# Performance work log

Hardware: AMD Instinct MI355X
Metric: run time of the kernel (lower is better)

The kernel has to match this reference:

```python
import jax, jax.numpy as jnp
import numpy as np
import math

B, T, C = 16, 1029, 1024
H, D = 16, 64  # n_heads, head_dim
NPH = NPW = 32  # 32x32 patch grid -> 1024 patch tokens
ROPE_BASE = 100.0


def _rope_cos_sin():
    # DINOv3 patch-center coordinates in [-1, 1]
    ch = (np.arange(0.5, NPH, dtype=np.float32) / NPH)
    cw = (np.arange(0.5, NPW, dtype=np.float32) / NPW)
    coords = np.stack(np.meshgrid(ch, cw, indexing='ij'), axis=-1).reshape(-1, 2)  # [N,2]
    coords = 2.0 * coords - 1.0
    inv_freq = 1.0 / ROPE_BASE ** np.arange(0, 1, 4.0 / D, dtype=np.float32)  # [D/4]
    angles = 2.0 * math.pi * coords[:, :, None] * inv_freq[None, None, :]  # [N,2,D/4]
    angles = angles.reshape(-1, D // 2)  # [N, D/2]
    angles = np.tile(angles, (1, 2))  # [N, D]
    return jnp.asarray(np.cos(angles)), jnp.asarray(np.sin(angles))


def setup_inputs() -> dict:
    key = jax.random.key(0)
    ks = jax.random.split(key, 6)
    s = 1.0 / math.sqrt(C)
    cos, sin = _rope_cos_sin()
    return {
        'x': jax.random.normal(ks[0], (B, T, C), jnp.float32),
        'Wqkv': jax.random.normal(ks[1], (C, 3 * C), jnp.float32) * s,
        'bqkv': jax.random.normal(ks[2], (3 * C,), jnp.float32) * 0.02,
        'Wout': jax.random.normal(ks[3], (C, C), jnp.float32) * s,
        'bout': jax.random.normal(ks[4], (C,), jnp.float32) * 0.02,
        'cos': cos,
        'sin': sin,
        'num_prefix': 5,  # 1 CLS + 4 registers
    }


def _rotate_half(t):
    t1, t2 = jnp.split(t, 2, axis=-1)
    return jnp.concatenate((-t2, t1), axis=-1)


def reference(x, Wqkv, bqkv, Wout, bout, cos, sin, num_prefix):
    Bx, Tx, Cx = x.shape
    qkv = x @ Wqkv + bqkv  # [B,T,3C]
    q, k, v = jnp.split(qkv, 3, axis=-1)
    to_heads = lambda t: t.reshape(Bx, Tx, H, D).transpose(0, 2, 1, 3)  # [B,H,T,D]
    q, k, v = to_heads(q), to_heads(k), to_heads(v)

    # RoPE on patch tokens only (skip CLS/register prefix)
    qp = q[:, :, num_prefix:] * cos + _rotate_half(q[:, :, num_prefix:]) * sin
    kp = k[:, :, num_prefix:] * cos + _rotate_half(k[:, :, num_prefix:]) * sin
    q = jnp.concatenate((q[:, :, :num_prefix], qp), axis=2)
    k = jnp.concatenate((k[:, :, :num_prefix], kp), axis=2)

    scale = 1.0 / math.sqrt(D)
    attn = jax.nn.softmax(jnp.einsum('bhqd,bhkd->bhqk', q, k) * scale, axis=-1)
    y = jnp.einsum('bhqk,bhkd->bhqd', attn, v)  # [B,H,T,D]
    y = y.transpose(0, 2, 1, 3).reshape(Bx, Tx, Cx)
    return y @ Wout + bout
```

## Files before the change

### kernel.cpp

```cpp
#include <hip/hip_runtime.h>
#include <hip/hip_bf16.h>
#include <stdint.h>

typedef __bf16 bf16;
typedef bf16 bf16x8 __attribute__((ext_vector_type(8)));
typedef bf16 bf16x4 __attribute__((ext_vector_type(4)));
typedef float f32x4 __attribute__((ext_vector_type(4)));

#define DEV static __device__ __forceinline__

constexpr int Bc = 16, Tc = 1029, Cc = 1024, Hc = 16, Dc = 64;
constexpr int KPAD = 1088;
constexpr int QPAD = 1152;
constexpr int MPAD = 16512;
constexpr int NKT  = KPAD / 64;
constexpr int NVT  = KPAD / 32;

DEV void gload16(void* lds_dst, const void* gsrc) {
  __builtin_amdgcn_global_load_lds(
      (const __attribute__((address_space(1))) void*)gsrc,
      (__attribute__((address_space(3))) void*)lds_dst, 16, 0, 0);
}

__global__ __launch_bounds__(256) void cast_x(const float* __restrict__ x,
                                              bf16* __restrict__ xb) {
  const size_t i = ((size_t)blockIdx.x * 256 + threadIdx.x) * 8;
  const int row = (int)(i >> 10);
  bf16x8 o = {};
  if (row < Bc * Tc) {
    const float4* p = (const float4*)(x + i);
    float4 a = p[0], b = p[1];
    o[0] = (bf16)a.x; o[1] = (bf16)a.y; o[2] = (bf16)a.z; o[3] = (bf16)a.w;
    o[4] = (bf16)b.x; o[5] = (bf16)b.y; o[6] = (bf16)b.z; o[7] = (bf16)b.w;
  }
  *(bf16x8*)(xb + i) = o;
}

__global__ __launch_bounds__(256) void transpose_cast(const float* __restrict__ W,
                                                      bf16* __restrict__ Wt,
                                                      int rows, int cols) {
  __shared__ float tile[32][33];
  const int c0 = blockIdx.x * 32;
  const int r0 = blockIdx.y * 32;
  const int tr = threadIdx.x >> 5;
  const int tc = threadIdx.x & 31;
#pragma unroll
  for (int j = 0; j < 4; ++j)
    tile[tr + j * 8][tc] = W[(size_t)(r0 + tr + j * 8) * cols + c0 + tc];
  __syncthreads();
#pragma unroll
  for (int j = 0; j < 4; ++j)
    Wt[(size_t)(c0 + tr + j * 8) * rows + r0 + tc] = (bf16)tile[tc][tr + j * 8];
}

template <bool OUT_BF16>
__global__ __launch_bounds__(256) void gemm_bt(const bf16* __restrict__ A,
                                               const bf16* __restrict__ Bt,
                                               const float* __restrict__ bias,
                                               void* __restrict__ Cout,
                                               int N, int K, int Mlim) {
  constexpr int BM = 128, BN = 128, BK = 32;
  __shared__ bf16 As[2][BM * BK];
  __shared__ bf16 Bs[2][BN * BK];
  const int tid  = threadIdx.x;
  const int lane = tid & 63;
  const int wave = tid >> 6;
  const int g = lane >> 4;
  const int c = lane & 15;
  const int m0 = blockIdx.y * BM;
  const int n0 = blockIdx.x * BN;
  const int wm = (wave >> 1) * 64;
  const int wn = (wave & 1) * 64;

  auto stage = [&](int buf, int k0) {
#pragma unroll
    for (int j = 0; j < 2; ++j) {
      int idx = j * 256 + tid;
      int row = idx >> 2, ch = idx & 3;
      int sc = ((ch ^ ((row >> 1) & 3)) << 4);
      gload16((char*)&As[buf][0] + idx * 16,
              (const char*)(A + (size_t)(m0 + row) * K + k0) + sc);
    }
#pragma unroll
    for (int j = 0; j < 2; ++j) {
      int idx = j * 256 + tid;
      int row = idx >> 2, ch = idx & 3;
      int sc = ((ch ^ ((row >> 1) & 3)) << 4);
      gload16((char*)&Bs[buf][0] + idx * 16,
              (const char*)(Bt + (size_t)(n0 + row) * K + k0) + sc);
    }
  };

  f32x4 acc[4][4] = {};
  stage(0, 0);
  __syncthreads();
  const int nk = K / BK;
  for (int kt = 0; kt < nk; ++kt) {
    const int buf = kt & 1;
    if (kt + 1 < nk) stage(buf ^ 1, (kt + 1) * BK);
    bf16x8 af[4], bfr[4];
#pragma unroll
    for (int i = 0; i < 4; ++i) {
      const int ra = wm + i * 16 + c;
      const int rb = wn + i * 16 + c;
      af[i]  = *(const bf16x8*)((const char*)&As[buf][0] + ra * 64 +
                                (((g ^ ((ra >> 1) & 3)) << 4)));
      bfr[i] = *(const bf16x8*)((const char*)&Bs[buf][0] + rb * 64 +
                                (((g ^ ((rb >> 1) & 3)) << 4)));
    }
#pragma unroll
    for (int i = 0; i < 4; ++i)
#pragma unroll
      for (int j = 0; j < 4; ++j)
        acc[i][j] = __builtin_amdgcn_mfma_f32_16x16x32_bf16(af[i], bfr[j], acc[i][j], 0, 0, 0);
    __syncthreads();
  }

#pragma unroll
  for (int i = 0; i < 4; ++i) {
    const int mb = m0 + wm + i * 16 + g * 4;
#pragma unroll
    for (int j = 0; j < 4; ++j) {
      const int n = n0 + wn + j * 16 + c;
      const float bv = bias[n];
#pragma unroll
      for (int r = 0; r < 4; ++r) {
        const int m = mb + r;
        if (m < Mlim) {
          float v = acc[i][j][r] + bv;
          if constexpr (OUT_BF16)
            ((bf16*)Cout)[(size_t)m * N + n] = (bf16)v;
          else
            ((float*)Cout)[(size_t)m * N + n] = v;
        }
      }
    }
  }
}

__global__ __launch_bounds__(256) void rope_qk(const bf16* __restrict__ qkv,
                                               const float* __restrict__ cosT,
                                               const float* __restrict__ sinT,
                                               const int* __restrict__ npfx_p,
                                               bf16* __restrict__ Qh,
                                               bf16* __restrict__ Kh) {
  const int bt = blockIdx.x;
  const int b = bt / QPAD, t = bt % QPAD;
  const int h  = threadIdx.x >> 4;
  const int d0 = (threadIdx.x & 15) * 4;
  const size_t qoff = (((size_t)(b * Hc + h)) * QPAD + t) * Dc + d0;
  const size_t koff = (((size_t)(b * Hc + h)) * KPAD + t) * Dc + d0;
  if (t >= Tc) {
    bf16x4 z = {};
    *(bf16x4*)(Qh + qoff) = z;
    if (t < KPAD) *(bf16x4*)(Kh + koff) = z;
    return;
  }
  const int npfx = *npfx_p;
  const size_t inb = ((size_t)b * Tc + t) * 3072 + h * Dc;
  bf16x4 qv = *(const bf16x4*)(qkv + inb + d0);
  bf16x4 kv = *(const bf16x4*)(qkv + inb + 1024 + d0);
  float q[4], k[4];
#pragma unroll
  for (int u = 0; u < 4; ++u) { q[u] = (float)qv[u]; k[u] = (float)kv[u]; }
  if (t >= npfx) {
    const int p  = t - npfx;
    const int dp = (d0 < 32) ? d0 + 32 : d0 - 32;
    const float sgn = (d0 < 32) ? -1.f : 1.f;
    bf16x4 qp = *(const bf16x4*)(qkv + inb + dp);
    bf16x4 kp = *(const bf16x4*)(qkv + inb + 1024 + dp);
    float4 csv = *(const float4*)(cosT + (size_t)p * Dc + d0);
    float4 snv = *(const float4*)(sinT + (size_t)p * Dc + d0);
    float cs[4] = {csv.x, csv.y, csv.z, csv.w};
    float sn[4] = {snv.x, snv.y, snv.z, snv.w};
#pragma unroll
    for (int u = 0; u < 4; ++u) {
      q[u] = q[u] * cs[u] + sgn * (float)qp[u] * sn[u];
      k[u] = k[u] * cs[u] + sgn * (float)kp[u] * sn[u];
    }
  }
  bf16x4 qo, ko;
#pragma unroll
  for (int u = 0; u < 4; ++u) {
    qo[u] = (bf16)(q[u] * 0.18033688f);
    ko[u] = (bf16)k[u];
  }
  *(bf16x4*)(Qh + qoff) = qo;
  *(bf16x4*)(Kh + koff) = ko;
}

__global__ __launch_bounds__(256) void vtrans(const bf16* __restrict__ qkv,
                                              bf16* __restrict__ Vt) {
  __shared__ bf16 lds[64][40];
  const int blk = blockIdx.x;
  const int tt = blk % NVT;
  const int bh = blk / NVT;
  const int b = bh >> 4, h = bh & 15;
  const int t0 = tt * 32;
  const int tl = threadIdx.x >> 3;
  const int ch = threadIdx.x & 7;
  bf16x8 v = {};
  const int t = t0 + tl;
  if (t < Tc)
    v = *(const bf16x8*)(qkv + ((size_t)b * Tc + t) * 3072 + 2048 + h * Dc + ch * 8);
#pragma unroll
  for (int u = 0; u < 8; ++u) lds[ch * 8 + u][tl] = v[u];
  __syncthreads();
  const int d  = threadIdx.x >> 2;
  const int tc = threadIdx.x & 3;
  bf16x8 o = *(const bf16x8*)&lds[d][tc * 8];
  *(bf16x8*)(Vt + ((size_t)bh * Dc + d) * KPAD + t0 + tc * 8) = o;
}

__global__ __launch_bounds__(256, 3) void attn4(const bf16* __restrict__ Qh,
                                                const bf16* __restrict__ Kh,
                                                const bf16* __restrict__ Vt,
                                                bf16* __restrict__ y2d) {
  __shared__ bf16 Ks[2][64 * 64];
  __shared__ bf16 Vs[2][64 * 64];
  __shared__ bf16 Ps[4][32 * 64];
  const int bh = blockIdx.y;
  const int b = bh >> 4, h = bh & 15;
  const int tid = threadIdx.x;
  const int w = tid >> 6, lane = tid & 63;
  const int g = lane >> 4, c = lane & 15;
  const int q0 = blockIdx.x * 128 + w * 32;
  const bf16* Qb = Qh + (size_t)bh * QPAD * Dc;
  const bf16* Kb = Kh + (size_t)bh * KPAD * Dc;
  const bf16* Vb = Vt + (size_t)bh * Dc * KPAD;
  char* Pw = (char*)&Ps[w][0];

  auto stage = [&](int buf, int k0) {
#pragma unroll
    for (int j = 0; j < 2; ++j) {
      int idx = j * 256 + tid;
      int row = idx >> 3;
      int scb = ((idx & 7) << 4) ^ ((row & 7) << 4);
      gload16((char*)&Ks[buf][0] + idx * 16,
              (const char*)(Kb + (size_t)(k0 + row) * 64) + scb);
    }
#pragma unroll
    for (int j = 0; j < 2; ++j) {
      int idx = j * 256 + tid;
      int row = idx >> 3;
      int scb = ((idx & 7) << 4) ^ ((row & 7) << 4);
      gload16((char*)&Vs[buf][0] + idx * 16,
              (const char*)(Vb + (size_t)row * KPAD + k0) + scb);
    }
  };

  bf16x8 qf[2][2];
#pragma unroll
  for (int fm = 0; fm < 2; ++fm)
#pragma unroll
    for (int kc = 0; kc < 2; ++kc)
      qf[fm][kc] = *(const bf16x8*)(Qb + (size_t)(q0 + fm * 16 + c) * Dc + kc * 32 + g * 8);

  bf16x8 ones;
#pragma unroll
  for (int u = 0; u < 8; ++u) ones[u] = (bf16)1.0f;

  float mrun[2] = {-1e30f, -1e30f}, lrun[2] = {0.f, 0.f};
  f32x4 oacc[2][4] = {};

  stage(0, 0);
  __syncthreads();

  for (int kt = 0; kt < NKT; ++kt) {
    const int buf = kt & 1;
    const int k0 = kt * 64;
    if (kt + 1 < NKT) stage(buf ^ 1, (kt + 1) * 64);

    f32x4 st[4][2] = {};
    __builtin_amdgcn_s_setprio(1);
#pragma unroll
    for (int fn = 0; fn < 4; ++fn) {
      const int row = fn * 16 + c;
      const int sw = (row & 7) << 4;
#pragma unroll
      for (int kc = 0; kc < 2; ++kc) {
        bf16x8 kf = *(const bf16x8*)((const char*)&Ks[buf][0] + row * 128 +
                                     ((kc * 64 + g * 16) ^ sw));
#pragma unroll
        for (int fm = 0; fm < 2; ++fm)
          st[fn][fm] = __builtin_amdgcn_mfma_f32_16x16x32_bf16(kf, qf[fm][kc], st[fn][fm], 0, 0, 0);
      }
    }
    __builtin_amdgcn_s_setprio(0);

    if (k0 + 64 > Tc) {
#pragma unroll
      for (int fn = 0; fn < 4; ++fn)
#pragma unroll
        for (int r = 0; r < 4; ++r)
          if (k0 + fn * 16 + g * 4 + r >= Tc) {
            st[fn][0][r] = -1e30f;
            st[fn][1][r] = -1e30f;
          }
    }

    float mx[2];
#pragma unroll
    for (int fm = 0; fm < 2; ++fm) {
      float m0 = fmaxf(fmaxf(st[0][fm][0], st[0][fm][1]), fmaxf(st[0][fm][2], st[0][fm][3]));
      float m1 = fmaxf(fmaxf(st[1][fm][0], st[1][fm][1]), fmaxf(st[1][fm][2], st[1][fm][3]));
      float m2 = fmaxf(fmaxf(st[2][fm][0], st[2][fm][1]), fmaxf(st[2][fm][2], st[2][fm][3]));
      float m3 = fmaxf(fmaxf(st[3][fm][0], st[3][fm][1]), fmaxf(st[3][fm][2], st[3][fm][3]));
      float m = fmaxf(fmaxf(m0, m1), fmaxf(m2, m3));
      m = fmaxf(m, __shfl_xor(m, 16));
      m = fmaxf(m, __shfl_xor(m, 32));
      mx[fm] = m;
    }
    const bool ok = (mx[0] - mrun[0] <= 11.f) && (mx[1] - mrun[1] <= 11.f);
    if (!__all(ok)) {
#pragma unroll
      for (int fm = 0; fm < 2; ++fm) {
        const float mnew = fmaxf(mrun[fm], mx[fm]);
        const float al = __builtin_amdgcn_exp2f(mrun[fm] - mnew);
        mrun[fm] = mnew;
        lrun[fm] *= al;
#pragma unroll
        for (int fd = 0; fd < 4; ++fd) oacc[fm][fd] *= al;
      }
    }
#pragma unroll
    for (int fm = 0; fm < 2; ++fm) {
      const int row = fm * 16 + c;
      const int sw = (row & 7) << 4;
#pragma unroll
      for (int fn = 0; fn < 4; ++fn) {
        bf16x4 pv;
#pragma unroll
        for (int r = 0; r < 4; ++r)
          pv[r] = (bf16)__builtin_amdgcn_exp2f(st[fn][fm][r] - mrun[fm]);
        *(bf16x4*)(Pw + row * 128 + ((fn * 32 + g * 8) ^ sw)) = pv;
      }
    }

    bf16x8 pf[2][2];
    f32x4 ps2[2] = {};
#pragma unroll
    for (int fm = 0; fm < 2; ++fm) {
      const int row = fm * 16 + c;
      const int sw = (row & 7) << 4;
#pragma unroll
      for (int kc = 0; kc < 2; ++kc) {
        pf[fm][kc] = *(const bf16x8*)(Pw + row * 128 + ((kc * 64 + g * 16) ^ sw));
        ps2[fm] = __builtin_amdgcn_mfma_f32_16x16x32_bf16(ones, pf[fm][kc], ps2[fm], 0, 0, 0);
      }
    }
    __builtin_amdgcn_s_setprio(1);
#pragma unroll
    for (int fd = 0; fd < 4; ++fd) {
      const int row = fd * 16 + c;
      const int sw = (row & 7) << 4;
#pragma unroll
      for (int kc = 0; kc < 2; ++kc) {
        bf16x8 vf = *(const bf16x8*)((const char*)&Vs[buf][0] + row * 128 +
                                     ((kc * 64 + g * 16) ^ sw));
#pragma unroll
        for (int fm = 0; fm < 2; ++fm)
          oacc[fm][fd] = __builtin_amdgcn_mfma_f32_16x16x32_bf16(vf, pf[fm][kc], oacc[fm][fd], 0, 0, 0);
      }
    }
    __builtin_amdgcn_s_setprio(0);
#pragma unroll
    for (int fm = 0; fm < 2; ++fm) lrun[fm] += ps2[fm][0];
    __syncthreads();
  }

#pragma unroll
  for (int fm = 0; fm < 2; ++fm) {
    const int trow = q0 + fm * 16 + c;
    if (trow < Tc) {
      const float inv = 1.f / lrun[fm];
#pragma unroll
      for (int fd = 0; fd < 4; ++fd) {
        bf16x4 ov;
#pragma unroll
        for (int r = 0; r < 4; ++r) ov[r] = (bf16)(oacc[fm][fd][r] * inv);
        *(bf16x4*)(y2d + ((size_t)b * Tc + trow) * Cc + h * Dc + fd * 16 + g * 4) = ov;
      }
    }
  }
}

extern "C" void kernel_launch(void* const* d_in, const int* in_sizes, int n_in,
                              void* d_out, int out_size, void* d_ws, size_t ws_size,
                              hipStream_t stream) {
  const float* x    = (const float*)d_in[0];
  const float* Wqkv = (const float*)d_in[1];
  const float* bqkv = (const float*)d_in[2];
  const float* Wout = (const float*)d_in[3];
  const float* bout = (const float*)d_in[4];
  const float* cosT = (const float*)d_in[5];
  const float* sinT = (const float*)d_in[6];
  const int*   npfx = (const int*)d_in[7];

  char* ws = (char*)d_ws;
  size_t off = 0;
  auto alloc = [&](size_t bytes) {
    char* p = ws + off;
    off = (off + bytes + 255) & ~(size_t)255;
    return p;
  };
  bf16* xb  = (bf16*)alloc((size_t)MPAD * 1024 * 2);
  bf16* Wt1 = (bf16*)alloc((size_t)3072 * 1024 * 2);
  bf16* Wt2 = (bf16*)alloc((size_t)1024 * 1024 * 2);
  bf16* qkv = (bf16*)alloc((size_t)MPAD * 3072 * 2);
  bf16* Qh  = (bf16*)alloc((size_t)256 * QPAD * 64 * 2);
  bf16* Kh  = (bf16*)alloc((size_t)256 * KPAD * 64 * 2);
  bf16* Vt  = (bf16*)alloc((size_t)256 * KPAD * 64 * 2);
  bf16* y2d = xb;
  if (off > ws_size) return;

  cast_x<<<dim3(MPAD * 1024 / 2048), dim3(256), 0, stream>>>(x, xb);
  transpose_cast<<<dim3(3072 / 32, 1024 / 32), dim3(256), 0, stream>>>(Wqkv, Wt1, 1024, 3072);
  transpose_cast<<<dim3(1024 / 32, 1024 / 32), dim3(256), 0, stream>>>(Wout, Wt2, 1024, 1024);
  gemm_bt<true><<<dim3(3072 / 128, MPAD / 128), dim3(256), 0, stream>>>(
      xb, Wt1, bqkv, (void*)qkv, 3072, 1024, MPAD);
  rope_qk<<<dim3(Bc * QPAD), dim3(256), 0, stream>>>(qkv, cosT, sinT, npfx, Qh, Kh);
  vtrans<<<dim3(256 * NVT), dim3(256), 0, stream>>>(qkv, Vt);
  attn4<<<dim3(QPAD / 128, 256), dim3(256), 0, stream>>>(Qh, Kh, Vt, y2d);
  gemm_bt<false><<<dim3(1024 / 128, MPAD / 128), dim3(256), 0, stream>>>(
      y2d, Wt2, bout, d_out, 1024, 1024, Bc * Tc);
}
```

Measured before the change: 391.7 us.

## Use 256x256 tiled 512-thread GEMM with XCD-aware block remap for QKV projection

Replaces the 128x128 QKV projection GEMM with a new kernel that uses 256x256 output tiles, BK=64, 8 waves, swizzled LDS staged via direct global-to-LDS loads, and a double-buffered pipeline. Block indices are remapped so consecutive tiles land on the same XCD, which should improve L2 reuse. MPAD is raised to a multiple of 256 so the padded rows fit, at the cost of extra padding work in cast_x. The larger tiles cut global and LDS traffic per FLOP but raise register and LDS pressure, which may lower occupancy.

After: 429.1 us. +9.5%, slower.

```diff
diff --git a/kernel.cpp b/kernel.cpp
--- a/kernel.cpp
+++ b/kernel.cpp
@@ -12,7 +12,7 @@
 constexpr int Bc = 16, Tc = 1029, Cc = 1024, Hc = 16, Dc = 64;
 constexpr int KPAD = 1088;
 constexpr int QPAD = 1152;
-constexpr int MPAD = 16512;
+constexpr int MPAD = 16640;
 constexpr int NKT  = KPAD / 64;
 constexpr int NVT  = KPAD / 32;
 
@@ -51,6 +51,129 @@
 #pragma unroll
   for (int j = 0; j < 4; ++j)
     Wt[(size_t)(c0 + tr + j * 8) * rows + r0 + tc] = (bf16)tile[tc][tr + j * 8];
+}
+
+template <bool OUT_BF16>
+__global__ __launch_bounds__(512, 2) void gemm256(const bf16* __restrict__ A,
+                                                  const bf16* __restrict__ Bt,
+                                                  const float* __restrict__ bias,
+                                                  void* __restrict__ Cout,
+                                                  int N, int K, int Mlim,
+                                                  int nblk_n) {
+  __shared__ bf16 As[2][256 * 64];
+  __shared__ bf16 Bs[2][256 * 64];
+  const int tid = threadIdx.x;
+  const int lane = tid & 63;
+  const int w = tid >> 6;
+  const int wm = w >> 2;
+  const int wn = w & 3;
+  const int g = lane >> 4, c = lane & 15;
+
+  const int nwg = gridDim.x;
+  const int orig = blockIdx.x;
+  const int q = nwg >> 3, r = nwg & 7;
+  const int xcd = orig & 7;
+  const int idx = (xcd < r ? xcd * (q + 1) : r * (q + 1) + (xcd - r) * q) + (orig >> 3);
+  const int m0 = (idx / nblk_n) * 256;
+  const int n0 = (idx % nblk_n) * 256;
+
+  auto stage = [&](int buf, int k0) {
+#pragma unroll
+    for (int j = 0; j < 4; ++j) {
+      const int id2 = j * 512 + tid;
+      const int row = id2 >> 3, ch = id2 & 7;
+      const int sc = (ch ^ (row & 7)) << 4;
+      gload16((char*)&As[buf][0] + id2 * 16,
+              (const char*)(A + (size_t)(m0 + row) * K + k0) + sc);
+    }
+#pragma unroll
+    for (int j = 0; j < 4; ++j) {
+      const int id2 = j * 512 + tid;
+      const int row = id2 >> 3, ch = id2 & 7;
+      const int sc = (ch ^ (row & 7)) << 4;
+      gload16((char*)&Bs[buf][0] + id2 * 16,
+              (const char*)(Bt + (size_t)(n0 + row) * K + k0) + sc);
+    }
+  };
+
+  f32x4 acc[8][4] = {};
+
+  stage(0, 0);
+  stage(1, 64);
+  asm volatile("s_waitcnt vmcnt(8)" ::: "memory");
+  __builtin_amdgcn_s_barrier();
+
+  const int nk = K / 64;
+  for (int kt = 0; kt < nk; ++kt) {
+    const int buf = kt & 1;
+
+    bf16x8 af[8][2], bq[4][2];
+#pragma unroll
+    for (int mi = 0; mi < 8; ++mi) {
+      const int row = wm * 128 + mi * 16 + c;
+#pragma unroll
+      for (int kc = 0; kc < 2; ++kc) {
+        const int chn = (kc * 4 + g) ^ (row & 7);
+        af[mi][kc] = *(const bf16x8*)((const char*)&As[buf][0] + row * 128 + chn * 16);
+      }
+    }
+#pragma unroll
+    for (int nj = 0; nj < 4; ++nj) {
+      const int row = wn * 64 + nj * 16 + c;
+#pragma unroll
+      for (int kc = 0; kc < 2; ++kc) {
+        const int chn = (kc * 4 + g) ^ (row & 7);
+        bq[nj][kc] = *(const bf16x8*)((const char*)&Bs[buf][0] + row * 128 + chn * 16);
+      }
+    }
+
+    asm volatile("s_waitcnt lgkmcnt(0)" ::: "memory");
+    __builtin_amdgcn_sched_barrier(0);
+    __builtin_amdgcn_s_barrier();
+    __builtin_amdgcn_sched_barrier(0);
+
+    if (kt + 2 < nk) stage(buf, (kt + 2) * 64);
+    __builtin_amdgcn_sched_barrier(0);
+
+    __builtin_amdgcn_s_setprio(1);
+#pragma unroll
+    for (int kc = 0; kc < 2; ++kc)
+#pragma unroll
+      for (int mi = 0; mi < 8; ++mi)
+#pragma unroll
+        for (int nj = 0; nj < 4; ++nj)
+          acc[mi][nj] = __builtin_amdgcn_mfma_f32_16x16x32_bf16(
+              af[mi][kc], bq[nj][kc], acc[mi][nj], 0, 0, 0);
+    __builtin_amdgcn_s_setprio(0);
+
+    if (kt + 2 < nk)
+      asm volatile("s_waitcnt vmcnt(8)" ::: "memory");
+    else
+      asm volatile("s_waitcnt vmcnt(0)" ::: "memory");
+    __builtin_amdgcn_sched_barrier(0);
+    __builtin_amdgcn_s_barrier();
+  }
+
+#pragma unroll
+  for (int mi = 0; mi < 8; ++mi) {
+    const int mb = m0 + wm * 128 + mi * 16 + g * 4;
+#pragma unroll
+    for (int nj = 0; nj < 4; ++nj) {
+      const int n = n0 + wn * 64 + nj * 16 + c;
+      const float bv = bias[n];
+#pragma unroll
+      for (int r2 = 0; r2 < 4; ++r2) {
+        const int m = mb + r2;
+        if (m < Mlim) {
+          const float v = acc[mi][nj][r2] + bv;
+          if constexpr (OUT_BF16)
+            ((bf16*)Cout)[(size_t)m * N + n] = (bf16)v;
+          else
+            ((float*)Cout)[(size_t)m * N + n] = v;
+        }
+      }
+    }
+  }
 }
 
 template <bool OUT_BF16>
@@ -417,8 +540,8 @@
   cast_x<<<dim3(MPAD * 1024 / 2048), dim3(256), 0, stream>>>(x, xb);
   transpose_cast<<<dim3(3072 / 32, 1024 / 32), dim3(256), 0, stream>>>(Wqkv, Wt1, 1024, 3072);
   transpose_cast<<<dim3(1024 / 32, 1024 / 32), dim3(256), 0, stream>>>(Wout, Wt2, 1024, 1024);
-  gemm_bt<true><<<dim3(3072 / 128, MPAD / 128), dim3(256), 0, stream>>>(
-      xb, Wt1, bqkv, (void*)qkv, 3072, 1024, MPAD);
+  gemm256<true><<<dim3((MPAD / 256) * (3072 / 256)), dim3(512), 0, stream>>>(
+      xb, Wt1, bqkv, (void*)qkv, 3072, 1024, MPAD, 3072 / 256);
   rope_qk<<<dim3(Bc * QPAD), dim3(256), 0, stream>>>(qkv, cosT, sinT, npfx, Qh, Kh);
   vtrans<<<dim3(256 * NVT), dim3(256), 0, stream>>>(qkv, Vt);
   attn4<<<dim3(QPAD / 128, 256), dim3(256), 0, stream>>>(Qh, Kh, Vt, y2d);
```
